# Performance work log

Hardware: AMD Instinct MI355X
Metric: run time of the kernel (lower is better)

Reference implementation:

```python
import jax, jax.numpy as jnp
import numpy as np

RANK = 8
ALPHA = 16.0
SCALING = ALPHA / RANK  # LoRA scaling alpha/rank
B, T, P, C = 8, 16, 197, 1024


def setup_inputs() -> dict:
    key = jax.random.key(0)
    k = jax.random.split(key, 8)
    hidden_states = jax.random.normal(k[0], (B, T, P, C), jnp.float32)
    frame_mask = jnp.ones((B, T), jnp.float32)
    # kaiming_uniform_(a=sqrt(5)) on an (out,in) Linear -> U(-1/sqrt(in), 1/sqrt(in))
    s_down = 1.0 / np.sqrt(C).astype(np.float32)
    down_w = jax.random.uniform(k[1], (RANK, C), jnp.float32, -s_down, s_down)
    # PyTorch LSTM default init: U(-1/sqrt(hidden), 1/sqrt(hidden)) for all params
    s_l = 1.0 / np.sqrt(RANK).astype(np.float32)
    w_ih = jax.random.uniform(k[2], (4 * RANK, RANK), jnp.float32, -s_l, s_l)
    w_hh = jax.random.uniform(k[3], (4 * RANK, RANK), jnp.float32, -s_l, s_l)
    b_ih = jax.random.uniform(k[4], (4 * RANK,), jnp.float32, -s_l, s_l)
    b_hh = jax.random.uniform(k[5], (4 * RANK,), jnp.float32, -s_l, s_l)
    # original zero-inits up; use small random so the reference output is non-trivial
    up_w = jax.random.normal(k[6], (C, RANK), jnp.float32) * 0.02
    return {
        "hidden_states": hidden_states,
        "num_frames": T,
        "frame_mask": frame_mask,
        "down_w": down_w,
        "w_ih": w_ih,
        "w_hh": w_hh,
        "b_ih": b_ih,
        "b_hh": b_hh,
        "up_w": up_w,
    }


def _lstm(x, w_ih, w_hh, b_ih, b_hh):
    """Single-layer unidirectional LSTM, PyTorch gate order (i,f,g,o).
    x: (T, N, R) time-major. Returns all hidden states (T, N, R)."""
    n, r = x.shape[1], w_hh.shape[1]
    bias = b_ih + b_hh

    def step(carry, x_t):
        h, c = carry
        gates = x_t @ w_ih.T + h @ w_hh.T + bias  # (N, 4R)
        i, f, g, o = jnp.split(gates, 4, axis=-1)
        c = jax.nn.sigmoid(f) * c + jax.nn.sigmoid(i) * jnp.tanh(g)
        h = jax.nn.sigmoid(o) * jnp.tanh(c)
        return (h, c), h

    init = (jnp.zeros((n, r), x.dtype), jnp.zeros((n, r), x.dtype))
    _, hs = jax.lax.scan(step, init, x)
    return hs


def reference(hidden_states, num_frames, frame_mask, down_w, w_ih, w_hh, b_ih, b_hh, up_w):
    b, t, p, c = hidden_states.shape
    assert t == num_frames
    # LoRA down: (B,T,P,C) x (R,C) -> (B,T,P,R)  (dropout is identity in eval)
    red = jnp.einsum('btpc,rc->btpr', hidden_states, down_w)
    red = red * frame_mask[:, :, None, None]
    # temporal LSTM over T, batch = B*P, in rank space
    seq = red.transpose(1, 0, 2, 3).reshape(t, b * p, -1)  # (T, B*P, R)
    hs = _lstm(seq, w_ih, w_hh, b_ih, b_hh)                # (T, B*P, R)
    out = hs.reshape(t, b, p, -1).transpose(1, 0, 2, 3)    # (B, T, P, R)
    out = out * frame_mask[:, :, None, None]
    # LoRA up + scaling: (B,T,P,R) x (C,R) -> (B,T,P,C)
    delta = jnp.einsum('btpr,or->btpo', out, up_w) * SCALING
    return delta
```

## Files before the change

kernel.cpp:

```cpp
#include <hip/hip_runtime.h>
#include <math.h>

#define BB 8
#define TT 16
#define PP 197
#define CC 1024
#define RR 8
#define NSEQ  (BB * PP)
#define LORA_SCALE 2.0f

__device__ __forceinline__ float sigf(float x) {
    x = fminf(fmaxf(x, -30.f), 30.f);
    return 1.0f / (1.0f + __expf(-x));
}
__device__ __forceinline__ float tanh_fast(float x) {
    x = fminf(fmaxf(x, -15.f), 15.f);
    float e = __expf(-2.0f * x);
    return (1.0f - e) / (1.0f + e);
}
__device__ __forceinline__ float dot4(const float4& a, const float4& b) {
    return a.x * b.x + a.y * b.y + a.z * b.z + a.w * b.w;
}

__global__ __launch_bounds__(64, 2) void k_fused(const float* __restrict__ hs,
                                                 const float* __restrict__ fm,
                                                 const float* __restrict__ dw,
                                                 const float* __restrict__ w_ih,
                                                 const float* __restrict__ w_hh,
                                                 const float* __restrict__ b_ih,
                                                 const float* __restrict__ b_hh,
                                                 const float* __restrict__ up,
                                                 float* __restrict__ out) {
    __shared__ float red_lds[TT][RR];
    __shared__ float h_lds[TT][RR];

    const int lane = threadIdx.x;
    const int seq  = blockIdx.x;
    const int b = seq / PP;
    const int p = seq - b * PP;
    const float* hsbase = hs + ((size_t)b * TT * PP + p) * CC;

    {
        float4 wreg[RR][4];
#pragma unroll
        for (int r = 0; r < RR; ++r)
#pragma unroll
            for (int k = 0; k < 4; ++k)
                wreg[r][k] = *(const float4*)(dw + r * CC + k * 256 + lane * 4);

        float4 buf[4][4];
#pragma unroll
        for (int t = 0; t < 4; ++t) {
            const float* rp = hsbase + (size_t)t * PP * CC;
#pragma unroll
            for (int k = 0; k < 4; ++k) buf[t][k] = *(const float4*)(rp + k * 256 + lane * 4);
        }
#pragma unroll
        for (int t = 0; t < TT; ++t) {
            const int s = t & 3;
            float acc[RR];
#pragma unroll
            for (int r = 0; r < RR; ++r) {
                float a = 0.f;
#pragma unroll
                for (int k = 0; k < 4; ++k) a += dot4(buf[s][k], wreg[r][k]);
                acc[r] = a;
            }
            if (t + 4 < TT) {
                const float* rp = hsbase + (size_t)(t + 4) * PP * CC;
#pragma unroll
                for (int k = 0; k < 4; ++k) buf[s][k] = *(const float4*)(rp + k * 256 + lane * 4);
            }
#pragma unroll
            for (int d = 32; d >= 1; d >>= 1)
#pragma unroll
                for (int r = 0; r < RR; ++r) acc[r] += __shfl_xor(acc[r], d, 64);
            if (lane == 0) {
                const float m = fm[b * TT + t];
                *(float4*)&red_lds[t][0] = make_float4(acc[0] * m, acc[1] * m, acc[2] * m, acc[3] * m);
                *(float4*)&red_lds[t][4] = make_float4(acc[4] * m, acc[5] * m, acc[6] * m, acc[7] * m);
            }
        }
    }

    {
        const int r = lane & 7;
        float wi[4][8], wh[4][8];
#pragma unroll
        for (int g = 0; g < 4; ++g)
#pragma unroll
            for (int j = 0; j < 8; ++j) {
                wi[g][j] = w_ih[(g * 8 + r) * 8 + j];
                wh[g][j] = w_hh[(g * 8 + r) * 8 + j];
            }
        const float bi = b_ih[r]      + b_hh[r];
        const float bf = b_ih[8 + r]  + b_hh[8 + r];
        const float bg = b_ih[16 + r] + b_hh[16 + r];
        const float bo = b_ih[24 + r] + b_hh[24 + r];

        float h = 0.f, c = 0.f;
#pragma unroll
        for (int t = 0; t < TT; ++t) {
            const float4 x0 = *(const float4*)&red_lds[t][0];
            const float4 x1 = *(const float4*)&red_lds[t][4];
            float gi = bi, gf = bf, gg = bg, go = bo;
            const float xs[8] = {x0.x, x0.y, x0.z, x0.w, x1.x, x1.y, x1.z, x1.w};
#pragma unroll
            for (int j = 0; j < 8; ++j) {
                const float hv = __shfl(h, j, 64);
                gi += wi[0][j] * xs[j] + wh[0][j] * hv;
                gf += wi[1][j] * xs[j] + wh[1][j] * hv;
                gg += wi[2][j] * xs[j] + wh[2][j] * hv;
                go += wi[3][j] * xs[j] + wh[3][j] * hv;
            }
            c = sigf(gf) * c + sigf(gi) * tanh_fast(gg);
            h = sigf(go) * tanh_fast(c);
            if (lane < 8) h_lds[t][lane] = h * fm[b * TT + t] * LORA_SCALE;
        }
    }

    {
        float4 u0[16], u1[16];
#pragma unroll
        for (int g = 0; g < 16; ++g) {
            const float* pp = up + (size_t)(g * 64 + lane) * RR;
            u0[g] = *(const float4*)(pp);
            u1[g] = *(const float4*)(pp + 4);
        }
        float* obase = out + ((size_t)b * TT * PP + p) * CC + lane;
#pragma unroll
        for (int t = 0; t < TT; ++t) {
            const float4 h0 = *(const float4*)&h_lds[t][0];
            const float4 h1 = *(const float4*)&h_lds[t][4];
            float* op = obase + (size_t)t * PP * CC;
#pragma unroll
            for (int g = 0; g < 16; ++g)
                op[g * 64] = dot4(h0, u0[g]) + dot4(h1, u1[g]);
        }
    }
}

extern "C" void kernel_launch(void* const* d_in, const int* in_sizes, int n_in,
                              void* d_out, int out_size, void* d_ws, size_t ws_size,
                              hipStream_t stream) {
    const float* hs  = (const float*)d_in[0];
    const float* fm  = (const float*)d_in[2];
    const float* dw  = (const float*)d_in[3];
    const float* wih = (const float*)d_in[4];
    const float* whh = (const float*)d_in[5];
    const float* bih = (const float*)d_in[6];
    const float* bhh = (const float*)d_in[7];
    const float* up  = (const float*)d_in[8];
    float* out = (float*)d_out;

    k_fused<<<NSEQ, 64, 0, stream>>>(hs, fm, dw, wih, whh, bih, bhh, up, out);
}
```

Measured before the change: 207.4 us.

## Split fused LoRA-LSTM kernel into down, LSTM and up kernels

Replaces the single fused kernel (one 64-thread block per sequence) with three kernels: a down-projection with many waves per block and the weights staged in shared memory, an LSTM kernel that runs 8 sequences per wave, and an up-projection that writes 4 rows per wave with float4 stores. Intermediates go through workspace buffers laid out time-major. The aim is higher occupancy and memory-level parallelism for the two bandwidth-bound projections, replacing tiny blocks whose serial LSTM phase left the memory system idle. The cost is two extra launches and a small round trip of intermediates through global memory.

```diff
diff --git a/kernel.cpp b/kernel.cpp
--- a/kernel.cpp
+++ b/kernel.cpp
@@ -7,6 +7,8 @@
 #define CC 1024
 #define RR 8
 #define NSEQ  (BB * PP)
+#define NROWS (BB * TT * PP)
+#define TP    (TT * PP)
 #define LORA_SCALE 2.0f
 
 __device__ __forceinline__ float sigf(float x) {
@@ -18,124 +20,185 @@
     float e = __expf(-2.0f * x);
     return (1.0f - e) / (1.0f + e);
 }
-__device__ __forceinline__ float dot4(const float4& a, const float4& b) {
+__device__ __forceinline__ float dot4(const float4 a, const float4 b) {
     return a.x * b.x + a.y * b.y + a.z * b.z + a.w * b.w;
 }
 
-__global__ __launch_bounds__(64, 2) void k_fused(const float* __restrict__ hs,
+__global__ __launch_bounds__(512, 4) void k_down(const float* __restrict__ hs,
+                                                 const float* __restrict__ dw,
                                                  const float* __restrict__ fm,
-                                                 const float* __restrict__ dw,
-                                                 const float* __restrict__ w_ih,
-                                                 const float* __restrict__ w_hh,
-                                                 const float* __restrict__ b_ih,
-                                                 const float* __restrict__ b_hh,
-                                                 const float* __restrict__ up,
-                                                 float* __restrict__ out) {
-    __shared__ float red_lds[TT][RR];
-    __shared__ float h_lds[TT][RR];
-
+                                                 float* __restrict__ red) {
+    __shared__ float4 w_lds[2048];
+    const int tid = threadIdx.x;
+#pragma unroll
+    for (int j = tid; j < 2048; j += 512) w_lds[j] = ((const float4*)dw)[j];
+    __syncthreads();
+
+    const int lane = tid & 63;
+    const int wv   = blockIdx.x * 8 + (tid >> 6);
+    const int row0 = wv * 2;
+
+    float4 xr[2][4];
+#pragma unroll
+    for (int i = 0; i < 2; ++i) {
+        const float* bp = hs + (size_t)(row0 + i) * CC;
+#pragma unroll
+        for (int k = 0; k < 4; ++k)
+            xr[i][k] = *(const float4*)(bp + k * 256 + lane * 4);
+    }
+
+    float acc[2][8];
+#pragma unroll
+    for (int i = 0; i < 2; ++i)
+#pragma unroll
+        for (int r = 0; r < 8; ++r) acc[i][r] = 0.f;
+
+#pragma unroll
+    for (int r = 0; r < 8; ++r)
+#pragma unroll
+        for (int k = 0; k < 4; ++k) {
+            const float4 w = w_lds[r * 256 + k * 64 + lane];
+            acc[0][r] += dot4(xr[0][k], w);
+            acc[1][r] += dot4(xr[1][k], w);
+        }
+
+#pragma unroll
+    for (int d = 32; d >= 1; d >>= 1)
+#pragma unroll
+        for (int i = 0; i < 2; ++i)
+#pragma unroll
+            for (int r = 0; r < 8; ++r)
+                acc[i][r] += __shfl_xor(acc[i][r], d, 64);
+
+    if (lane == 0) {
+#pragma unroll
+        for (int i = 0; i < 2; ++i) {
+            const int row = row0 + i;
+            const int b = row / TP;
+            const int rem = row - b * TP;
+            const int t = rem / PP;
+            const int p = rem - t * PP;
+            const float m = fm[b * TT + t];
+            float* op = red + ((size_t)t * NSEQ + b * PP + p) * RR;
+            *(float4*)op       = make_float4(acc[i][0] * m, acc[i][1] * m,
+                                             acc[i][2] * m, acc[i][3] * m);
+            *(float4*)(op + 4) = make_float4(acc[i][4] * m, acc[i][5] * m,
+                                             acc[i][6] * m, acc[i][7] * m);
+        }
+    }
+}
+
+__global__ __launch_bounds__(64, 1) void k_lstm(const float* __restrict__ red,
+                                                const float* __restrict__ wihp,
+                                                const float* __restrict__ whhp,
+                                                const float* __restrict__ bihp,
+                                                const float* __restrict__ bhhp,
+                                                const float* __restrict__ fm,
+                                                float* __restrict__ hout) {
     const int lane = threadIdx.x;
-    const int seq  = blockIdx.x;
-    const int b = seq / PP;
-    const int p = seq - b * PP;
-    const float* hsbase = hs + ((size_t)b * TT * PP + p) * CC;
-
-    {
-        float4 wreg[RR][4];
-#pragma unroll
-        for (int r = 0; r < RR; ++r)
-#pragma unroll
-            for (int k = 0; k < 4; ++k)
-                wreg[r][k] = *(const float4*)(dw + r * CC + k * 256 + lane * 4);
-
-        float4 buf[4][4];
-#pragma unroll
-        for (int t = 0; t < 4; ++t) {
-            const float* rp = hsbase + (size_t)t * PP * CC;
-#pragma unroll
-            for (int k = 0; k < 4; ++k) buf[t][k] = *(const float4*)(rp + k * 256 + lane * 4);
-        }
-#pragma unroll
-        for (int t = 0; t < TT; ++t) {
-            const int s = t & 3;
-            float acc[RR];
-#pragma unroll
-            for (int r = 0; r < RR; ++r) {
-                float a = 0.f;
-#pragma unroll
-                for (int k = 0; k < 4; ++k) a += dot4(buf[s][k], wreg[r][k]);
-                acc[r] = a;
+    const int sub  = lane >> 3;
+    const int r    = lane & 7;
+    const int seq  = blockIdx.x * 8 + sub;
+    const int b    = seq / PP;
+
+    float wi[4][8], wh[4][8], bias[4];
+#pragma unroll
+    for (int g = 0; g < 4; ++g) {
+        const float* wp = wihp + (g * 8 + r) * 8;
+        float4 a = *(const float4*)wp, b4 = *(const float4*)(wp + 4);
+        wi[g][0] = a.x;  wi[g][1] = a.y;  wi[g][2] = a.z;  wi[g][3] = a.w;
+        wi[g][4] = b4.x; wi[g][5] = b4.y; wi[g][6] = b4.z; wi[g][7] = b4.w;
+        const float* hp = whhp + (g * 8 + r) * 8;
+        float4 c4 = *(const float4*)hp, d4 = *(const float4*)(hp + 4);
+        wh[g][0] = c4.x; wh[g][1] = c4.y; wh[g][2] = c4.z; wh[g][3] = c4.w;
+        wh[g][4] = d4.x; wh[g][5] = d4.y; wh[g][6] = d4.z; wh[g][7] = d4.w;
+        bias[g] = bihp[g * 8 + r] + bhhp[g * 8 + r];
+    }
+
+    float msk[TT];
+#pragma unroll
+    for (int t = 0; t < TT; ++t) msk[t] = fm[b * TT + t];
+
+    const float* xp = red + (size_t)seq * RR;
+    float4 xa = *(const float4*)xp;
+    float4 xb = *(const float4*)(xp + 4);
+
+    float h = 0.f, c = 0.f;
+#pragma unroll
+    for (int t = 0; t < TT; ++t) {
+        float4 na, nb;
+        if (t < TT - 1) {
+            const float* np = red + ((size_t)(t + 1) * NSEQ + seq) * RR;
+            na = *(const float4*)np;
+            nb = *(const float4*)(np + 4);
+        }
+        const float xs[8] = {xa.x, xa.y, xa.z, xa.w, xb.x, xb.y, xb.z, xb.w};
+        float gi = bias[0], gf = bias[1], gg = bias[2], go = bias[3];
+#pragma unroll
+        for (int j = 0; j < 8; ++j) {
+            const float hv = __shfl(h, j, 8);
+            gi += wi[0][j] * xs[j] + wh[0][j] * hv;
+            gf += wi[1][j] * xs[j] + wh[1][j] * hv;
+            gg += wi[2][j] * xs[j] + wh[2][j] * hv;
+            go += wi[3][j] * xs[j] + wh[3][j] * hv;
+        }
+        c = sigf(gf) * c + sigf(gi) * tanh_fast(gg);
+        h = sigf(go) * tanh_fast(c);
+        hout[((size_t)t * NSEQ + seq) * RR + r] = h * msk[t] * LORA_SCALE;
+        if (t < TT - 1) { xa = na; xb = nb; }
+    }
+}
+
+__global__ __launch_bounds__(512, 4) void k_up(const float* __restrict__ hsq,
+                                               const float* __restrict__ up,
+                                               float* __restrict__ out) {
+    __shared__ float upT[8][1024];
+    const int tid = threadIdx.x;
+#pragma unroll
+    for (int c0 = tid; c0 < CC; c0 += 512) {
+        float4 a  = *(const float4*)(up + (size_t)c0 * RR);
+        float4 b4 = *(const float4*)(up + (size_t)c0 * RR + 4);
+        upT[0][c0] = a.x;  upT[1][c0] = a.y;  upT[2][c0] = a.z;  upT[3][c0] = a.w;
+        upT[4][c0] = b4.x; upT[5][c0] = b4.y; upT[6][c0] = b4.z; upT[7][c0] = b4.w;
+    }
+    __syncthreads();
+
+    const int lane = tid & 63;
+    const int wv   = blockIdx.x * 8 + (tid >> 6);
+    const int row0 = wv * 4;
+
+    float hv[4][8];
+#pragma unroll
+    for (int i = 0; i < 4; ++i) {
+        const int row = row0 + i;
+        const int b = row / TP;
+        const int rem = row - b * TP;
+        const int t = rem / PP;
+        const int p = rem - t * PP;
+        const float* hp = hsq + ((size_t)t * NSEQ + b * PP + p) * RR;
+        float4 a  = *(const float4*)hp;
+        float4 b4 = *(const float4*)(hp + 4);
+        hv[i][0] = a.x;  hv[i][1] = a.y;  hv[i][2] = a.z;  hv[i][3] = a.w;
+        hv[i][4] = b4.x; hv[i][5] = b4.y; hv[i][6] = b4.z; hv[i][7] = b4.w;
+    }
+
+#pragma unroll
+    for (int g4 = 0; g4 < 4; ++g4) {
+        float4 w[8];
+#pragma unroll
+        for (int r = 0; r < 8; ++r)
+            w[r] = *(const float4*)&upT[r][g4 * 256 + lane * 4];
+#pragma unroll
+        for (int i = 0; i < 4; ++i) {
+            float4 o = make_float4(0.f, 0.f, 0.f, 0.f);
+#pragma unroll
+            for (int r = 0; r < 8; ++r) {
+                o.x += hv[i][r] * w[r].x;
+                o.y += hv[i][r] * w[r].y;
+                o.z += hv[i][r] * w[r].z;
+                o.w += hv[i][r] * w[r].w;
             }
-            if (t + 4 < TT) {
-                const float* rp = hsbase + (size_t)(t + 4) * PP * CC;
-#pragma unroll
-                for (int k = 0; k < 4; ++k) buf[s][k] = *(const float4*)(rp + k * 256 + lane * 4);
-            }
-#pragma unroll
-            for (int d = 32; d >= 1; d >>= 1)
-#pragma unroll
-                for (int r = 0; r < RR; ++r) acc[r] += __shfl_xor(acc[r], d, 64);
-            if (lane == 0) {
-                const float m = fm[b * TT + t];
-                *(float4*)&red_lds[t][0] = make_float4(acc[0] * m, acc[1] * m, acc[2] * m, acc[3] * m);
-                *(float4*)&red_lds[t][4] = make_float4(acc[4] * m, acc[5] * m, acc[6] * m, acc[7] * m);
-            }
-        }
-    }
-
-    {
-        const int r = lane & 7;
-        float wi[4][8], wh[4][8];
-#pragma unroll
-        for (int g = 0; g < 4; ++g)
-#pragma unroll
-            for (int j = 0; j < 8; ++j) {
-                wi[g][j] = w_ih[(g * 8 + r) * 8 + j];
-                wh[g][j] = w_hh[(g * 8 + r) * 8 + j];
-            }
-        const float bi = b_ih[r]      + b_hh[r];
-        const float bf = b_ih[8 + r]  + b_hh[8 + r];
-        const float bg = b_ih[16 + r] + b_hh[16 + r];
-        const float bo = b_ih[24 + r] + b_hh[24 + r];
-
-        float h = 0.f, c = 0.f;
-#pragma unroll
-        for (int t = 0; t < TT; ++t) {
-            const float4 x0 = *(const float4*)&red_lds[t][0];
-            const float4 x1 = *(const float4*)&red_lds[t][4];
-            float gi = bi, gf = bf, gg = bg, go = bo;
-            const float xs[8] = {x0.x, x0.y, x0.z, x0.w, x1.x, x1.y, x1.z, x1.w};
-#pragma unroll
-            for (int j = 0; j < 8; ++j) {
-                const float hv = __shfl(h, j, 64);
-                gi += wi[0][j] * xs[j] + wh[0][j] * hv;
-                gf += wi[1][j] * xs[j] + wh[1][j] * hv;
-                gg += wi[2][j] * xs[j] + wh[2][j] * hv;
-                go += wi[3][j] * xs[j] + wh[3][j] * hv;
-            }
-            c = sigf(gf) * c + sigf(gi) * tanh_fast(gg);
-            h = sigf(go) * tanh_fast(c);
-            if (lane < 8) h_lds[t][lane] = h * fm[b * TT + t] * LORA_SCALE;
-        }
-    }
-
-    {
-        float4 u0[16], u1[16];
-#pragma unroll
-        for (int g = 0; g < 16; ++g) {
-            const float* pp = up + (size_t)(g * 64 + lane) * RR;
-            u0[g] = *(const float4*)(pp);
-            u1[g] = *(const float4*)(pp + 4);
-        }
-        float* obase = out + ((size_t)b * TT * PP + p) * CC + lane;
-#pragma unroll
-        for (int t = 0; t < TT; ++t) {
-            const float4 h0 = *(const float4*)&h_lds[t][0];
-            const float4 h1 = *(const float4*)&h_lds[t][4];
-            float* op = obase + (size_t)t * PP * CC;
-#pragma unroll
-            for (int g = 0; g < 16; ++g)
-                op[g * 64] = dot4(h0, u0[g]) + dot4(h1, u1[g]);
+            *(float4*)(out + (size_t)(row0 + i) * CC + g4 * 256 + lane * 4) = o;
         }
     }
 }
@@ -153,5 +216,10 @@
     const float* up  = (const float*)d_in[8];
     float* out = (float*)d_out;
 
-    k_fused<<<NSEQ, 64, 0, stream>>>(hs, fm, dw, wih, whh, bih, bhh, up, out);
-}
+    float* red_ws = (float*)d_ws;
+    float* h_ws   = red_ws + (1 << 18);
+
+    k_down<<<NSEQ, 512, 0, stream>>>(hs, dw, fm, red_ws);
+    k_lstm<<<NSEQ / 8, 64, 0, stream>>>(red_ws, wih, whh, bih, bhh, fm, h_ws);
+    k_up<<<NROWS / 32, 512, 0, stream>>>(h_ws, up, out);
+}
```

New measurement: 216.8 us. +4.5%, slower.

## Split each sequence across four waves for down/up projections and parallelize LSTM gates

Applied to the files above, without the earlier changes.

Each block now uses four wavefronts instead of one. Each wave handles four timesteps of the down-projection and of the up-projection, so more loads are in flight per sequence. The LSTM step now computes one gate row per lane across 32 lanes and exchanges activations with shuffles, instead of each lane computing all four gates serially. The up-projection now writes float4 stores. The cost is two block barriers, with three of the four waves idle during the serial LSTM phase.

```diff
diff --git a/kernel.cpp b/kernel.cpp
--- a/kernel.cpp
+++ b/kernel.cpp
@@ -18,124 +18,136 @@
     float e = __expf(-2.0f * x);
     return (1.0f - e) / (1.0f + e);
 }
-__device__ __forceinline__ float dot4(const float4& a, const float4& b) {
+__device__ __forceinline__ float dot4(const float4 a, const float4 b) {
     return a.x * b.x + a.y * b.y + a.z * b.z + a.w * b.w;
 }
 
-__global__ __launch_bounds__(64, 2) void k_fused(const float* __restrict__ hs,
-                                                 const float* __restrict__ fm,
-                                                 const float* __restrict__ dw,
-                                                 const float* __restrict__ w_ih,
-                                                 const float* __restrict__ w_hh,
-                                                 const float* __restrict__ b_ih,
-                                                 const float* __restrict__ b_hh,
-                                                 const float* __restrict__ up,
-                                                 float* __restrict__ out) {
+__global__ __launch_bounds__(256, 6) void k_fused2(const float* __restrict__ hs,
+                                                   const float* __restrict__ fm,
+                                                   const float* __restrict__ dw,
+                                                   const float* __restrict__ w_ih,
+                                                   const float* __restrict__ w_hh,
+                                                   const float* __restrict__ b_ih,
+                                                   const float* __restrict__ b_hh,
+                                                   const float* __restrict__ up,
+                                                   float* __restrict__ out) {
     __shared__ float red_lds[TT][RR];
     __shared__ float h_lds[TT][RR];
 
-    const int lane = threadIdx.x;
+    const int tid  = threadIdx.x;
+    const int lane = tid & 63;
+    const int wv   = tid >> 6;
     const int seq  = blockIdx.x;
-    const int b = seq / PP;
-    const int p = seq - b * PP;
+    const int b    = seq / PP;
+    const int p    = seq - b * PP;
     const float* hsbase = hs + ((size_t)b * TT * PP + p) * CC;
 
-    {
-        float4 wreg[RR][4];
+#pragma unroll
+    for (int batch = 0; batch < 2; ++batch) {
+        const int t0 = wv * 4 + batch * 2;
+        float4 xr[2][4];
+#pragma unroll
+        for (int i = 0; i < 2; ++i) {
+            const float* rp = hsbase + (size_t)(t0 + i) * PP * CC;
+#pragma unroll
+            for (int k = 0; k < 4; ++k)
+                xr[i][k] = *(const float4*)(rp + k * 256 + lane * 4);
+        }
+        float acc[2][RR];
+#pragma unroll
+        for (int i = 0; i < 2; ++i)
+#pragma unroll
+            for (int r = 0; r < RR; ++r) acc[i][r] = 0.f;
 #pragma unroll
         for (int r = 0; r < RR; ++r)
 #pragma unroll
-            for (int k = 0; k < 4; ++k)
-                wreg[r][k] = *(const float4*)(dw + r * CC + k * 256 + lane * 4);
-
-        float4 buf[4][4];
-#pragma unroll
-        for (int t = 0; t < 4; ++t) {
-            const float* rp = hsbase + (size_t)t * PP * CC;
-#pragma unroll
-            for (int k = 0; k < 4; ++k) buf[t][k] = *(const float4*)(rp + k * 256 + lane * 4);
-        }
-#pragma unroll
-        for (int t = 0; t < TT; ++t) {
-            const int s = t & 3;
-            float acc[RR];
-#pragma unroll
-            for (int r = 0; r < RR; ++r) {
-                float a = 0.f;
-#pragma unroll
-                for (int k = 0; k < 4; ++k) a += dot4(buf[s][k], wreg[r][k]);
-                acc[r] = a;
-            }
-            if (t + 4 < TT) {
-                const float* rp = hsbase + (size_t)(t + 4) * PP * CC;
-#pragma unroll
-                for (int k = 0; k < 4; ++k) buf[s][k] = *(const float4*)(rp + k * 256 + lane * 4);
+            for (int k = 0; k < 4; ++k) {
+                const float4 w = *(const float4*)(dw + r * CC + k * 256 + lane * 4);
+                acc[0][r] += dot4(xr[0][k], w);
+                acc[1][r] += dot4(xr[1][k], w);
             }
 #pragma unroll
-            for (int d = 32; d >= 1; d >>= 1)
+        for (int d = 32; d >= 1; d >>= 1)
 #pragma unroll
-                for (int r = 0; r < RR; ++r) acc[r] += __shfl_xor(acc[r], d, 64);
-            if (lane == 0) {
-                const float m = fm[b * TT + t];
-                *(float4*)&red_lds[t][0] = make_float4(acc[0] * m, acc[1] * m, acc[2] * m, acc[3] * m);
-                *(float4*)&red_lds[t][4] = make_float4(acc[4] * m, acc[5] * m, acc[6] * m, acc[7] * m);
+            for (int i = 0; i < 2; ++i)
+#pragma unroll
+                for (int r = 0; r < RR; ++r)
+                    acc[i][r] += __shfl_xor(acc[i][r], d, 64);
+        if (lane == 0) {
+#pragma unroll
+            for (int i = 0; i < 2; ++i) {
+                const float m = fm[b * TT + t0 + i];
+                *(float4*)&red_lds[t0 + i][0] = make_float4(acc[i][0] * m, acc[i][1] * m,
+                                                            acc[i][2] * m, acc[i][3] * m);
+                *(float4*)&red_lds[t0 + i][4] = make_float4(acc[i][4] * m, acc[i][5] * m,
+                                                            acc[i][6] * m, acc[i][7] * m);
             }
         }
     }
+    __syncthreads();
 
-    {
-        const int r = lane & 7;
-        float wi[4][8], wh[4][8];
-#pragma unroll
-        for (int g = 0; g < 4; ++g)
-#pragma unroll
-            for (int j = 0; j < 8; ++j) {
-                wi[g][j] = w_ih[(g * 8 + r) * 8 + j];
-                wh[g][j] = w_hh[(g * 8 + r) * 8 + j];
-            }
-        const float bi = b_ih[r]      + b_hh[r];
-        const float bf = b_ih[8 + r]  + b_hh[8 + r];
-        const float bg = b_ih[16 + r] + b_hh[16 + r];
-        const float bo = b_ih[24 + r] + b_hh[24 + r];
+    if (wv == 0) {
+        const int idx = lane & 31;
+        const int r   = idx & 7;
+        const bool isG = (idx >> 3) == 2;
+        float wr[8], whv[8];
+        {
+            const float* wip = w_ih + idx * 8;
+            float4 a = *(const float4*)wip, b4 = *(const float4*)(wip + 4);
+            wr[0] = a.x;  wr[1] = a.y;  wr[2] = a.z;  wr[3] = a.w;
+            wr[4] = b4.x; wr[5] = b4.y; wr[6] = b4.z; wr[7] = b4.w;
+            const float* whp = w_hh + idx * 8;
+            float4 c4 = *(const float4*)whp, d4 = *(const float4*)(whp + 4);
+            whv[0] = c4.x; whv[1] = c4.y; whv[2] = c4.z; whv[3] = c4.w;
+            whv[4] = d4.x; whv[5] = d4.y; whv[6] = d4.z; whv[7] = d4.w;
+        }
+        const float bias = b_ih[idx] + b_hh[idx];
 
         float h = 0.f, c = 0.f;
 #pragma unroll
         for (int t = 0; t < TT; ++t) {
             const float4 x0 = *(const float4*)&red_lds[t][0];
             const float4 x1 = *(const float4*)&red_lds[t][4];
-            float gi = bi, gf = bf, gg = bg, go = bo;
             const float xs[8] = {x0.x, x0.y, x0.z, x0.w, x1.x, x1.y, x1.z, x1.w};
+            float gv = bias;
 #pragma unroll
-            for (int j = 0; j < 8; ++j) {
-                const float hv = __shfl(h, j, 64);
-                gi += wi[0][j] * xs[j] + wh[0][j] * hv;
-                gf += wi[1][j] * xs[j] + wh[1][j] * hv;
-                gg += wi[2][j] * xs[j] + wh[2][j] * hv;
-                go += wi[3][j] * xs[j] + wh[3][j] * hv;
-            }
-            c = sigf(gf) * c + sigf(gi) * tanh_fast(gg);
-            h = sigf(go) * tanh_fast(c);
+            for (int j = 0; j < 8; ++j) gv += wr[j] * xs[j];
+#pragma unroll
+            for (int j = 0; j < 8; ++j) gv += whv[j] * __shfl(h, j, 64);
+            const float sg = sigf(gv);
+            const float tg = tanh_fast(gv);
+            const float a  = isG ? tg : sg;
+            const float fa = __shfl(a,  8 + r, 64);
+            const float ga = __shfl(a, 16 + r, 64);
+            const float oa = __shfl(a, 24 + r, 64);
+            c = fa * c + a * ga;
+            h = oa * tanh_fast(c);
             if (lane < 8) h_lds[t][lane] = h * fm[b * TT + t] * LORA_SCALE;
         }
     }
+    __syncthreads();
 
-    {
-        float4 u0[16], u1[16];
+    float* obase = out + ((size_t)b * TT * PP + p) * CC;
 #pragma unroll
-        for (int g = 0; g < 16; ++g) {
-            const float* pp = up + (size_t)(g * 64 + lane) * RR;
-            u0[g] = *(const float4*)(pp);
-            u1[g] = *(const float4*)(pp + 4);
+    for (int g4 = 0; g4 < 4; ++g4) {
+        const float* wp = up + (size_t)(g4 * 256 + lane * 4) * RR;
+        float4 wA[4], wB[4];
+#pragma unroll
+        for (int c4 = 0; c4 < 4; ++c4) {
+            wA[c4] = *(const float4*)(wp + c4 * RR);
+            wB[c4] = *(const float4*)(wp + c4 * RR + 4);
         }
-        float* obase = out + ((size_t)b * TT * PP + p) * CC + lane;
 #pragma unroll
-        for (int t = 0; t < TT; ++t) {
+        for (int i = 0; i < 4; ++i) {
+            const int t = wv * 4 + i;
             const float4 h0 = *(const float4*)&h_lds[t][0];
             const float4 h1 = *(const float4*)&h_lds[t][4];
-            float* op = obase + (size_t)t * PP * CC;
-#pragma unroll
-            for (int g = 0; g < 16; ++g)
-                op[g * 64] = dot4(h0, u0[g]) + dot4(h1, u1[g]);
+            float4 o;
+            o.x = dot4(h0, wA[0]) + dot4(h1, wB[0]);
+            o.y = dot4(h0, wA[1]) + dot4(h1, wB[1]);
+            o.z = dot4(h0, wA[2]) + dot4(h1, wB[2]);
+            o.w = dot4(h0, wA[3]) + dot4(h1, wB[3]);
+            *(float4*)(obase + (size_t)t * PP * CC + g4 * 256 + lane * 4) = o;
         }
     }
 }
@@ -153,5 +165,7 @@
     const float* up  = (const float*)d_in[8];
     float* out = (float*)d_out;
 
-    k_fused<<<NSEQ, 64, 0, stream>>>(hs, fm, dw, wih, whh, bih, bhh, up, out);
+    (void)d_ws; (void)ws_size;
+
+    k_fused2<<<NSEQ, 256, 0, stream>>>(hs, fm, dw, wih, whh, bih, bhh, up, out);
 }
```

New measurement: 395.3 us. +90.6%, slower.
